# Performance work log

Hardware: AMD Instinct MI355X
Metric: run time of the kernel (lower is better)

## Reference

```python
import jax, jax.numpy as jnp
import numpy as np


def setup_inputs() -> dict:
    key = jax.random.key(0)
    k1, k2 = jax.random.split(key)
    B, C, N = 8, 64, 65536
    features = jax.random.normal(k1, (B, C, N), dtype=jnp.float32)
    coords = jax.random.uniform(k2, (B, 3, N), dtype=jnp.float32)  # normalized xyz in [0,1)
    return {"features": features, "coords": coords, "resolution": 32}


def reference(features, coords, resolution):
    """avg_voxelize: quantize coords to an r^3 grid, scatter-average features.

    features: [B, C, N] float; coords: [B, 3, N] float in [0,1].
    Returns (vox [B, C, r, r, r], norm_coords [B, 3, N]).
    """
    r = resolution
    B, C, N = features.shape
    norm_coords = jnp.clip(coords * r, 0, r - 1)                 # [B, 3, N]
    vox = jnp.round(norm_coords).astype(jnp.int32)               # [B, 3, N]
    # linear voxel index per point: x*r^2 + y*r + z
    idx = (vox[:, 0] * r + vox[:, 1]) * r + vox[:, 2]            # [B, N]
    flat_idx = (idx + jnp.arange(B, dtype=jnp.int32)[:, None] * (r * r * r)).reshape(-1)  # [B*N]
    feats = features.transpose(0, 2, 1).reshape(B * N, C)        # [B*N, C]
    num_seg = B * r * r * r
    sums = jax.ops.segment_sum(feats, flat_idx, num_segments=num_seg)            # [B*r^3, C]
    cnt = jax.ops.segment_sum(jnp.ones((B * N,), features.dtype), flat_idx,
                              num_segments=num_seg)                              # [B*r^3]
    avg = sums / jnp.maximum(cnt, 1.0)[:, None]
    out = avg.reshape(B, r, r, r, C).transpose(0, 4, 1, 2, 3)    # [B, C, r, r, r]
    return out, norm_coords
```

## Files before the change

kernel.cpp:

```cpp
#include <hip/hip_runtime.h>
#include <hip/hip_bf16.h>


#define BB 8
#define CC 64
#define NN 65536
#define RR 32
#define R3 (RR * RR * RR)
#define OFFSTRIDE (R3 + 1)

__global__ __launch_bounds__(256) void points_kernel(
    const float* __restrict__ coords,
    float* __restrict__ norm_out,
    unsigned int* __restrict__ cnt,
    unsigned int* __restrict__ packed)
{
    int gid = blockIdx.x * 256 + threadIdx.x;
    int b = gid >> 16;
    int n = gid & (NN - 1);

    const float* cb = coords + (size_t)b * 3 * NN;
    float x = cb[n];
    float y = cb[NN + n];
    float z = cb[2 * NN + n];

    float nx = fminf(fmaxf(x * (float)RR, 0.0f), (float)(RR - 1));
    float ny = fminf(fmaxf(y * (float)RR, 0.0f), (float)(RR - 1));
    float nz = fminf(fmaxf(z * (float)RR, 0.0f), (float)(RR - 1));

    float* nb = norm_out + (size_t)b * 3 * NN;
    nb[n] = nx;
    nb[NN + n] = ny;
    nb[2 * NN + n] = nz;

    int vx = (int)rintf(nx);
    int vy = (int)rintf(ny);
    int vz = (int)rintf(nz);
    unsigned int idx = (unsigned int)((vx * RR + vy) * RR + vz);

    unsigned int rank = atomicAdd(&cnt[b * R3 + idx], 1u);
    packed[gid] = (idx << 17) | rank;
}

__global__ __launch_bounds__(1024) void scan_kernel(
    const unsigned int* __restrict__ cnt,
    unsigned int* __restrict__ off)
{
    int b = blockIdx.x;
    int t = threadIdx.x;
    const unsigned int* c = cnt + (size_t)b * R3;
    unsigned int* o = off + (size_t)b * OFFSTRIDE;

    unsigned int loc[32];
    unsigned int s = 0;
    #pragma unroll
    for (int k = 0; k < 32; k++) { loc[k] = c[t * 32 + k]; s += loc[k]; }

    __shared__ unsigned int aux[1024];
    aux[t] = s;
    __syncthreads();
    for (int d = 1; d < 1024; d <<= 1) {
        unsigned int v = (t >= d) ? aux[t - d] : 0u;
        __syncthreads();
        aux[t] += v;
        __syncthreads();
    }
    unsigned int run = (t == 0) ? 0u : aux[t - 1];
    #pragma unroll
    for (int k = 0; k < 32; k++) { o[t * 32 + k] = run; run += loc[k]; }
    if (t == 1023) o[R3] = run;
}

__global__ __launch_bounds__(256) void pos_kernel(
    const unsigned int* __restrict__ packed,
    const unsigned int* __restrict__ off,
    unsigned int* __restrict__ pos)
{
    int gid = blockIdx.x * 256 + threadIdx.x;
    int b = gid >> 16;
    unsigned int pk = packed[gid];
    unsigned int ix = pk >> 17;
    unsigned int rk = pk & 0x1FFFFu;
    pos[gid] = off[(size_t)b * OFFSTRIDE + ix] + rk;
}

__global__ __launch_bounds__(1024) void gather_kernel(
    const float* __restrict__ feats,
    const unsigned int* __restrict__ pos,
    const unsigned int* __restrict__ off,
    float* __restrict__ out)
{
    __shared__ __hip_bfloat16 srt[NN];

    int c = blockIdx.x;
    int b = blockIdx.y;
    int t = threadIdx.x;

    const float* f = feats + ((size_t)b * CC + c) * NN;
    const unsigned int* P = pos + (size_t)b * NN;

    for (int n0 = t * 4; n0 < NN; n0 += 1024 * 4) {
        float4 fv = *(const float4*)(f + n0);
        uint4 pv = *(const uint4*)(P + n0);
        srt[pv.x] = __float2bfloat16(fv.x);
        srt[pv.y] = __float2bfloat16(fv.y);
        srt[pv.z] = __float2bfloat16(fv.z);
        srt[pv.w] = __float2bfloat16(fv.w);
    }
    __syncthreads();

    const unsigned int* O = off + (size_t)b * OFFSTRIDE;
    float* ob = out + ((size_t)b * CC + c) * R3;
    for (int j = 0; j < 32; j++) {
        int v = t + j * 1024;
        unsigned int s0 = O[v];
        unsigned int s1 = O[v + 1];
        float s = 0.0f;
        for (unsigned int p = s0; p < s1; p++) s += __bfloat162float(srt[p]);
        float cf = (float)(s1 - s0);
        ob[v] = s / fmaxf(cf, 1.0f);
    }
}

extern "C" void kernel_launch(void* const* d_in, const int* in_sizes, int n_in,
                              void* d_out, int out_size, void* d_ws, size_t ws_size,
                              hipStream_t stream) {
    const float* feats  = (const float*)d_in[0];
    const float* coords = (const float*)d_in[1];

    float* out_vox  = (float*)d_out;
    float* out_norm = out_vox + (size_t)BB * CC * R3;

    char* ws = (char*)d_ws;
    unsigned int* cnt    = (unsigned int*)ws;
    unsigned int* off    = (unsigned int*)(ws + 1048576);
    unsigned int* packed = (unsigned int*)(ws + 1048576 + 1048608);
    unsigned int* pos    = (unsigned int*)(ws + 1048576 + 1048608 + 2097152);

    hipMemsetAsync(cnt, 0, (size_t)BB * R3 * sizeof(unsigned int), stream);

    points_kernel<<<(BB * NN) / 256, 256, 0, stream>>>(coords, out_norm, cnt, packed);
    scan_kernel<<<BB, 1024, 0, stream>>>(cnt, off);
    pos_kernel<<<(BB * NN) / 256, 256, 0, stream>>>(packed, off, pos);
    gather_kernel<<<dim3(CC, BB), 1024, 0, stream>>>(feats, pos, off, out_vox);
}
```

Baseline: 289.3 us.

## Replace counting-sort pipeline with LDS float atomic scatter-add per channel

Drops the scan and position kernels and the sorted bf16 staging buffer. Points now emit 16-bit voxel indices and bump counts, and the gather kernel accumulates features into a 128KB shared float array with unsafe atomic adds before dividing by the counts. The points kernel is also vectorized to four points per thread. This removes two launches and the serial per-voxel loops, and restores fp32 accumulation. In exchange it relies on LDS atomic throughput, and the 128KB shared allocation may limit occupancy to one block per CU.

```diff
diff --git a/kernel.cpp b/kernel.cpp
--- a/kernel.cpp
+++ b/kernel.cpp
@@ -1,5 +1,4 @@
 #include <hip/hip_runtime.h>
-#include <hip/hip_bf16.h>
 
 
 #define BB 8
@@ -7,118 +6,109 @@
 #define NN 65536
 #define RR 32
 #define R3 (RR * RR * RR)
-#define OFFSTRIDE (R3 + 1)
 
 __global__ __launch_bounds__(256) void points_kernel(
     const float* __restrict__ coords,
     float* __restrict__ norm_out,
     unsigned int* __restrict__ cnt,
-    unsigned int* __restrict__ packed)
+    unsigned short* __restrict__ idx_out)
 {
     int gid = blockIdx.x * 256 + threadIdx.x;
-    int b = gid >> 16;
-    int n = gid & (NN - 1);
+    int b  = gid >> 14;
+    int n4 = (gid & 16383) * 4;
 
     const float* cb = coords + (size_t)b * 3 * NN;
-    float x = cb[n];
-    float y = cb[NN + n];
-    float z = cb[2 * NN + n];
+    float4 x = *(const float4*)(cb + n4);
+    float4 y = *(const float4*)(cb + NN + n4);
+    float4 z = *(const float4*)(cb + 2 * NN + n4);
 
-    float nx = fminf(fmaxf(x * (float)RR, 0.0f), (float)(RR - 1));
-    float ny = fminf(fmaxf(y * (float)RR, 0.0f), (float)(RR - 1));
-    float nz = fminf(fmaxf(z * (float)RR, 0.0f), (float)(RR - 1));
+    float4 nx, ny, nz;
+    nx.x = fminf(fmaxf(x.x * 32.f, 0.f), 31.f);
+    nx.y = fminf(fmaxf(x.y * 32.f, 0.f), 31.f);
+    nx.z = fminf(fmaxf(x.z * 32.f, 0.f), 31.f);
+    nx.w = fminf(fmaxf(x.w * 32.f, 0.f), 31.f);
+    ny.x = fminf(fmaxf(y.x * 32.f, 0.f), 31.f);
+    ny.y = fminf(fmaxf(y.y * 32.f, 0.f), 31.f);
+    ny.z = fminf(fmaxf(y.z * 32.f, 0.f), 31.f);
+    ny.w = fminf(fmaxf(y.w * 32.f, 0.f), 31.f);
+    nz.x = fminf(fmaxf(z.x * 32.f, 0.f), 31.f);
+    nz.y = fminf(fmaxf(z.y * 32.f, 0.f), 31.f);
+    nz.z = fminf(fmaxf(z.z * 32.f, 0.f), 31.f);
+    nz.w = fminf(fmaxf(z.w * 32.f, 0.f), 31.f);
 
     float* nb = norm_out + (size_t)b * 3 * NN;
-    nb[n] = nx;
-    nb[NN + n] = ny;
-    nb[2 * NN + n] = nz;
+    *(float4*)(nb + n4)          = nx;
+    *(float4*)(nb + NN + n4)     = ny;
+    *(float4*)(nb + 2 * NN + n4) = nz;
 
-    int vx = (int)rintf(nx);
-    int vy = (int)rintf(ny);
-    int vz = (int)rintf(nz);
-    unsigned int idx = (unsigned int)((vx * RR + vy) * RR + vz);
+    int i0 = ((int)rintf(nx.x) << 10) | ((int)rintf(ny.x) << 5) | (int)rintf(nz.x);
+    int i1 = ((int)rintf(nx.y) << 10) | ((int)rintf(ny.y) << 5) | (int)rintf(nz.y);
+    int i2 = ((int)rintf(nx.z) << 10) | ((int)rintf(ny.z) << 5) | (int)rintf(nz.z);
+    int i3 = ((int)rintf(nx.w) << 10) | ((int)rintf(ny.w) << 5) | (int)rintf(nz.w);
 
-    unsigned int rank = atomicAdd(&cnt[b * R3 + idx], 1u);
-    packed[gid] = (idx << 17) | rank;
-}
+    unsigned short* ib = idx_out + (size_t)b * NN;
+    *(ushort4*)(ib + n4) = make_ushort4((unsigned short)i0, (unsigned short)i1,
+                                        (unsigned short)i2, (unsigned short)i3);
 
-__global__ __launch_bounds__(1024) void scan_kernel(
-    const unsigned int* __restrict__ cnt,
-    unsigned int* __restrict__ off)
-{
-    int b = blockIdx.x;
-    int t = threadIdx.x;
-    const unsigned int* c = cnt + (size_t)b * R3;
-    unsigned int* o = off + (size_t)b * OFFSTRIDE;
-
-    unsigned int loc[32];
-    unsigned int s = 0;
-    #pragma unroll
-    for (int k = 0; k < 32; k++) { loc[k] = c[t * 32 + k]; s += loc[k]; }
-
-    __shared__ unsigned int aux[1024];
-    aux[t] = s;
-    __syncthreads();
-    for (int d = 1; d < 1024; d <<= 1) {
-        unsigned int v = (t >= d) ? aux[t - d] : 0u;
-        __syncthreads();
-        aux[t] += v;
-        __syncthreads();
-    }
-    unsigned int run = (t == 0) ? 0u : aux[t - 1];
-    #pragma unroll
-    for (int k = 0; k < 32; k++) { o[t * 32 + k] = run; run += loc[k]; }
-    if (t == 1023) o[R3] = run;
-}
-
-__global__ __launch_bounds__(256) void pos_kernel(
-    const unsigned int* __restrict__ packed,
-    const unsigned int* __restrict__ off,
-    unsigned int* __restrict__ pos)
-{
-    int gid = blockIdx.x * 256 + threadIdx.x;
-    int b = gid >> 16;
-    unsigned int pk = packed[gid];
-    unsigned int ix = pk >> 17;
-    unsigned int rk = pk & 0x1FFFFu;
-    pos[gid] = off[(size_t)b * OFFSTRIDE + ix] + rk;
+    unsigned int* cc = cnt + (size_t)b * R3;
+    atomicAdd(&cc[i0], 1u);
+    atomicAdd(&cc[i1], 1u);
+    atomicAdd(&cc[i2], 1u);
+    atomicAdd(&cc[i3], 1u);
 }
 
 __global__ __launch_bounds__(1024) void gather_kernel(
     const float* __restrict__ feats,
-    const unsigned int* __restrict__ pos,
-    const unsigned int* __restrict__ off,
+    const unsigned short* __restrict__ idx,
+    const unsigned int* __restrict__ cnt,
     float* __restrict__ out)
 {
-    __shared__ __hip_bfloat16 srt[NN];
+    __shared__ float acc[R3];
 
     int c = blockIdx.x;
     int b = blockIdx.y;
     int t = threadIdx.x;
 
-    const float* f = feats + ((size_t)b * CC + c) * NN;
-    const unsigned int* P = pos + (size_t)b * NN;
-
-    for (int n0 = t * 4; n0 < NN; n0 += 1024 * 4) {
-        float4 fv = *(const float4*)(f + n0);
-        uint4 pv = *(const uint4*)(P + n0);
-        srt[pv.x] = __float2bfloat16(fv.x);
-        srt[pv.y] = __float2bfloat16(fv.y);
-        srt[pv.z] = __float2bfloat16(fv.z);
-        srt[pv.w] = __float2bfloat16(fv.w);
+    #pragma unroll
+    for (int j = 0; j < 8; j++) {
+        *(float4*)(acc + (t + j * 1024) * 4) = make_float4(0.f, 0.f, 0.f, 0.f);
     }
     __syncthreads();
 
-    const unsigned int* O = off + (size_t)b * OFFSTRIDE;
+    const float* f = feats + ((size_t)b * CC + c) * NN;
+    const unsigned short* I = idx + (size_t)b * NN;
+
+    #pragma unroll
+    for (int it = 0; it < 8; it++) {
+        int n0 = (t + it * 1024) * 8;
+        float4 f0 = *(const float4*)(f + n0);
+        float4 f1 = *(const float4*)(f + n0 + 4);
+        ushort4 v0 = *(const ushort4*)(I + n0);
+        ushort4 v1 = *(const ushort4*)(I + n0 + 4);
+        unsafeAtomicAdd(&acc[v0.x], f0.x);
+        unsafeAtomicAdd(&acc[v0.y], f0.y);
+        unsafeAtomicAdd(&acc[v0.z], f0.z);
+        unsafeAtomicAdd(&acc[v0.w], f0.w);
+        unsafeAtomicAdd(&acc[v1.x], f1.x);
+        unsafeAtomicAdd(&acc[v1.y], f1.y);
+        unsafeAtomicAdd(&acc[v1.z], f1.z);
+        unsafeAtomicAdd(&acc[v1.w], f1.w);
+    }
+    __syncthreads();
+
+    const unsigned int* cb = cnt + (size_t)b * R3;
     float* ob = out + ((size_t)b * CC + c) * R3;
-    for (int j = 0; j < 32; j++) {
-        int v = t + j * 1024;
-        unsigned int s0 = O[v];
-        unsigned int s1 = O[v + 1];
-        float s = 0.0f;
-        for (unsigned int p = s0; p < s1; p++) s += __bfloat162float(srt[p]);
-        float cf = (float)(s1 - s0);
-        ob[v] = s / fmaxf(cf, 1.0f);
+    #pragma unroll
+    for (int j = 0; j < 8; j++) {
+        int v = (t + j * 1024) * 4;
+        float4 s = *(const float4*)(acc + v);
+        uint4 cv = *(const uint4*)(cb + v);
+        float4 o;
+        o.x = __fdividef(s.x, fmaxf((float)cv.x, 1.f));
+        o.y = __fdividef(s.y, fmaxf((float)cv.y, 1.f));
+        o.z = __fdividef(s.z, fmaxf((float)cv.z, 1.f));
+        o.w = __fdividef(s.w, fmaxf((float)cv.w, 1.f));
+        *(float4*)(ob + v) = o;
     }
 }
 
@@ -132,15 +122,11 @@
     float* out_norm = out_vox + (size_t)BB * CC * R3;
 
     char* ws = (char*)d_ws;
-    unsigned int* cnt    = (unsigned int*)ws;
-    unsigned int* off    = (unsigned int*)(ws + 1048576);
-    unsigned int* packed = (unsigned int*)(ws + 1048576 + 1048608);
-    unsigned int* pos    = (unsigned int*)(ws + 1048576 + 1048608 + 2097152);
+    unsigned int*   cnt = (unsigned int*)ws;
+    unsigned short* idx = (unsigned short*)(ws + 1048576);
 
     hipMemsetAsync(cnt, 0, (size_t)BB * R3 * sizeof(unsigned int), stream);
 
-    points_kernel<<<(BB * NN) / 256, 256, 0, stream>>>(coords, out_norm, cnt, packed);
-    scan_kernel<<<BB, 1024, 0, stream>>>(cnt, off);
-    pos_kernel<<<(BB * NN) / 256, 256, 0, stream>>>(packed, off, pos);
-    gather_kernel<<<dim3(CC, BB), 1024, 0, stream>>>(feats, pos, off, out_vox);
+    points_kernel<<<(BB * NN / 4) / 256, 256, 0, stream>>>(coords, out_norm, cnt, idx);
+    gather_kernel<<<dim3(CC, BB), 1024, 0, stream>>>(feats, idx, cnt, out_vox);
 }
```

Measured after the change: 363.7 us. +25.7%, slower.

## Replace global atomic histogram with per-block LDS histograms and packed subhistograms

Applied to the files above, without the earlier changes.

Points are binned into per-block shared-memory histograms (4 sub-blocks per batch), and the counts are written as packed 16-bit pairs. This replaces the global atomics and the memset. The scan merges the sub-histograms into per-sub-block prefix offsets, and the pos kernel rewrites packed entries in place, vectorized. The goal is to cut global atomic contention and launch/memset overhead. The trade-off is that points_kernel now runs only 32 blocks, which reduces parallelism in that phase.

```diff
diff --git a/kernel.cpp b/kernel.cpp
--- a/kernel.cpp
+++ b/kernel.cpp
@@ -7,57 +7,110 @@
 #define NN 65536
 #define RR 32
 #define R3 (RR * RR * RR)
-#define OFFSTRIDE (R3 + 1)
-
-__global__ __launch_bounds__(256) void points_kernel(
+#define NSUB 4
+#define PTS (NN / NSUB)
+#define HWORDS (R3 / 2)
+
+__global__ __launch_bounds__(1024) void points_kernel(
     const float* __restrict__ coords,
     float* __restrict__ norm_out,
-    unsigned int* __restrict__ cnt,
-    unsigned int* __restrict__ packed)
-{
-    int gid = blockIdx.x * 256 + threadIdx.x;
-    int b = gid >> 16;
-    int n = gid & (NN - 1);
+    unsigned int* __restrict__ packed,
+    unsigned int* __restrict__ ghist)
+{
+    __shared__ unsigned int hist[R3];
+    int blk = blockIdx.x;
+    int b = blk >> 2;
+    int s = blk & 3;
+    int t = threadIdx.x;
+
+    #pragma unroll
+    for (int k = 0; k < 8; k++)
+        *(uint4*)(hist + 4 * (t + k * 1024)) = make_uint4(0u, 0u, 0u, 0u);
+    __syncthreads();
 
     const float* cb = coords + (size_t)b * 3 * NN;
-    float x = cb[n];
-    float y = cb[NN + n];
-    float z = cb[2 * NN + n];
-
-    float nx = fminf(fmaxf(x * (float)RR, 0.0f), (float)(RR - 1));
-    float ny = fminf(fmaxf(y * (float)RR, 0.0f), (float)(RR - 1));
-    float nz = fminf(fmaxf(z * (float)RR, 0.0f), (float)(RR - 1));
-
     float* nb = norm_out + (size_t)b * 3 * NN;
-    nb[n] = nx;
-    nb[NN + n] = ny;
-    nb[2 * NN + n] = nz;
-
-    int vx = (int)rintf(nx);
-    int vy = (int)rintf(ny);
-    int vz = (int)rintf(nz);
-    unsigned int idx = (unsigned int)((vx * RR + vy) * RR + vz);
-
-    unsigned int rank = atomicAdd(&cnt[b * R3 + idx], 1u);
-    packed[gid] = (idx << 17) | rank;
+    unsigned int* pb = packed + (size_t)b * NN;
+
+    #pragma unroll
+    for (int p = 0; p < 4; p++) {
+        int n = s * PTS + (t + p * 1024) * 4;
+        float4 x = *(const float4*)(cb + n);
+        float4 y = *(const float4*)(cb + NN + n);
+        float4 z = *(const float4*)(cb + 2 * NN + n);
+
+        float4 nx, ny, nz;
+        nx.x = fminf(fmaxf(x.x * 32.f, 0.f), 31.f);
+        nx.y = fminf(fmaxf(x.y * 32.f, 0.f), 31.f);
+        nx.z = fminf(fmaxf(x.z * 32.f, 0.f), 31.f);
+        nx.w = fminf(fmaxf(x.w * 32.f, 0.f), 31.f);
+        ny.x = fminf(fmaxf(y.x * 32.f, 0.f), 31.f);
+        ny.y = fminf(fmaxf(y.y * 32.f, 0.f), 31.f);
+        ny.z = fminf(fmaxf(y.z * 32.f, 0.f), 31.f);
+        ny.w = fminf(fmaxf(y.w * 32.f, 0.f), 31.f);
+        nz.x = fminf(fmaxf(z.x * 32.f, 0.f), 31.f);
+        nz.y = fminf(fmaxf(z.y * 32.f, 0.f), 31.f);
+        nz.z = fminf(fmaxf(z.z * 32.f, 0.f), 31.f);
+        nz.w = fminf(fmaxf(z.w * 32.f, 0.f), 31.f);
+
+        *(float4*)(nb + n)          = nx;
+        *(float4*)(nb + NN + n)     = ny;
+        *(float4*)(nb + 2 * NN + n) = nz;
+
+        int i0 = ((int)rintf(nx.x) << 10) | ((int)rintf(ny.x) << 5) | (int)rintf(nz.x);
+        int i1 = ((int)rintf(nx.y) << 10) | ((int)rintf(ny.y) << 5) | (int)rintf(nz.y);
+        int i2 = ((int)rintf(nx.z) << 10) | ((int)rintf(ny.z) << 5) | (int)rintf(nz.z);
+        int i3 = ((int)rintf(nx.w) << 10) | ((int)rintf(ny.w) << 5) | (int)rintf(nz.w);
+
+        unsigned int r0 = atomicAdd(&hist[i0], 1u);
+        unsigned int r1 = atomicAdd(&hist[i1], 1u);
+        unsigned int r2 = atomicAdd(&hist[i2], 1u);
+        unsigned int r3 = atomicAdd(&hist[i3], 1u);
+
+        *(uint4*)(pb + n) = make_uint4(((unsigned)i0 << 14) | r0,
+                                       ((unsigned)i1 << 14) | r1,
+                                       ((unsigned)i2 << 14) | r2,
+                                       ((unsigned)i3 << 14) | r3);
+    }
+    __syncthreads();
+
+    unsigned int* gh = ghist + (size_t)blk * HWORDS;
+    #pragma unroll
+    for (int k = 0; k < 16; k++) {
+        int w = t + k * 1024;
+        uint2 u = *(const uint2*)(hist + 2 * w);
+        gh[w] = u.x | (u.y << 16);
+    }
 }
 
 __global__ __launch_bounds__(1024) void scan_kernel(
-    const unsigned int* __restrict__ cnt,
+    unsigned int* __restrict__ ghist,
     unsigned int* __restrict__ off)
 {
     int b = blockIdx.x;
     int t = threadIdx.x;
-    const unsigned int* c = cnt + (size_t)b * R3;
-    unsigned int* o = off + (size_t)b * OFFSTRIDE;
-
-    unsigned int loc[32];
-    unsigned int s = 0;
-    #pragma unroll
-    for (int k = 0; k < 32; k++) { loc[k] = c[t * 32 + k]; s += loc[k]; }
+
+    unsigned int cnt_lo[16], cnt_hi[16];
+    unsigned int tsum = 0;
+    #pragma unroll
+    for (int k = 0; k < 16; k++) {
+        int w = t * 16 + k;
+        unsigned int lo = 0, hi = 0;
+        #pragma unroll
+        for (int s = 0; s < NSUB; s++) {
+            unsigned int* p = ghist + (size_t)(b * NSUB + s) * HWORDS + w;
+            unsigned int u = *p;
+            *p = lo | (hi << 16);
+            lo += u & 0xFFFFu;
+            hi += u >> 16;
+        }
+        cnt_lo[k] = lo;
+        cnt_hi[k] = hi;
+        tsum += lo + hi;
+    }
 
     __shared__ unsigned int aux[1024];
-    aux[t] = s;
+    aux[t] = tsum;
     __syncthreads();
     for (int d = 1; d < 1024; d <<= 1) {
         unsigned int v = (t >= d) ? aux[t - d] : 0u;
@@ -66,22 +119,52 @@
         __syncthreads();
     }
     unsigned int run = (t == 0) ? 0u : aux[t - 1];
-    #pragma unroll
-    for (int k = 0; k < 32; k++) { o[t * 32 + k] = run; run += loc[k]; }
-    if (t == 1023) o[R3] = run;
+
+    unsigned int* O = off + (size_t)b * R3;
+    #pragma unroll
+    for (int k = 0; k < 16; k++) {
+        int v = t * 32 + 2 * k;
+        *(uint2*)(O + v) = make_uint2(run, run + cnt_lo[k]);
+        run += cnt_lo[k] + cnt_hi[k];
+    }
 }
 
 __global__ __launch_bounds__(256) void pos_kernel(
-    const unsigned int* __restrict__ packed,
+    unsigned int* __restrict__ packed,
     const unsigned int* __restrict__ off,
-    unsigned int* __restrict__ pos)
+    const unsigned int* __restrict__ ghist)
 {
     int gid = blockIdx.x * 256 + threadIdx.x;
-    int b = gid >> 16;
-    unsigned int pk = packed[gid];
-    unsigned int ix = pk >> 17;
-    unsigned int rk = pk & 0x1FFFFu;
-    pos[gid] = off[(size_t)b * OFFSTRIDE + ix] + rk;
+    int b  = gid >> 14;
+    int n4 = (gid & 16383) * 4;
+    int s  = n4 >> 14;
+
+    unsigned int* pb = packed + (size_t)b * NN + n4;
+    const unsigned int* O = off + (size_t)b * R3;
+    const unsigned int* G = ghist + (size_t)(b * NSUB + s) * HWORDS;
+
+    uint4 pk = *(uint4*)pb;
+    {
+        unsigned v = pk.x >> 14, r = pk.x & 16383u;
+        unsigned u = G[v >> 1];
+        pk.x = O[v] + ((v & 1) ? (u >> 16) : (u & 0xFFFFu)) + r;
+    }
+    {
+        unsigned v = pk.y >> 14, r = pk.y & 16383u;
+        unsigned u = G[v >> 1];
+        pk.y = O[v] + ((v & 1) ? (u >> 16) : (u & 0xFFFFu)) + r;
+    }
+    {
+        unsigned v = pk.z >> 14, r = pk.z & 16383u;
+        unsigned u = G[v >> 1];
+        pk.z = O[v] + ((v & 1) ? (u >> 16) : (u & 0xFFFFu)) + r;
+    }
+    {
+        unsigned v = pk.w >> 14, r = pk.w & 16383u;
+        unsigned u = G[v >> 1];
+        pk.w = O[v] + ((v & 1) ? (u >> 16) : (u & 0xFFFFu)) + r;
+    }
+    *(uint4*)pb = pk;
 }
 
 __global__ __launch_bounds__(1024) void gather_kernel(
@@ -109,16 +192,15 @@
     }
     __syncthreads();
 
-    const unsigned int* O = off + (size_t)b * OFFSTRIDE;
+    const unsigned int* O = off + (size_t)b * R3;
     float* ob = out + ((size_t)b * CC + c) * R3;
     for (int j = 0; j < 32; j++) {
         int v = t + j * 1024;
         unsigned int s0 = O[v];
-        unsigned int s1 = O[v + 1];
+        unsigned int s1 = (v < R3 - 1) ? O[v + 1] : (unsigned)NN;
         float s = 0.0f;
         for (unsigned int p = s0; p < s1; p++) s += __bfloat162float(srt[p]);
-        float cf = (float)(s1 - s0);
-        ob[v] = s / fmaxf(cf, 1.0f);
+        ob[v] = __fdividef(s, fmaxf((float)(s1 - s0), 1.0f));
     }
 }
 
@@ -132,15 +214,12 @@
     float* out_norm = out_vox + (size_t)BB * CC * R3;
 
     char* ws = (char*)d_ws;
-    unsigned int* cnt    = (unsigned int*)ws;
-    unsigned int* off    = (unsigned int*)(ws + 1048576);
-    unsigned int* packed = (unsigned int*)(ws + 1048576 + 1048608);
-    unsigned int* pos    = (unsigned int*)(ws + 1048576 + 1048608 + 2097152);
-
-    hipMemsetAsync(cnt, 0, (size_t)BB * R3 * sizeof(unsigned int), stream);
-
-    points_kernel<<<(BB * NN) / 256, 256, 0, stream>>>(coords, out_norm, cnt, packed);
-    scan_kernel<<<BB, 1024, 0, stream>>>(cnt, off);
-    pos_kernel<<<(BB * NN) / 256, 256, 0, stream>>>(packed, off, pos);
-    gather_kernel<<<dim3(CC, BB), 1024, 0, stream>>>(feats, pos, off, out_vox);
-}
+    unsigned int* ghist  = (unsigned int*)ws;
+    unsigned int* packed = (unsigned int*)(ws + (2 << 20));
+    unsigned int* off    = (unsigned int*)(ws + (4 << 20));
+
+    points_kernel<<<BB * NSUB, 1024, 0, stream>>>(coords, out_norm, packed, ghist);
+    scan_kernel<<<BB, 1024, 0, stream>>>(ghist, off);
+    pos_kernel<<<(BB * NN / 4) / 256, 256, 0, stream>>>(packed, off, ghist);
+    gather_kernel<<<dim3(CC, BB), 1024, 0, stream>>>(feats, packed, off, out_vox);
+}
```

After: 286.9 us. No clear change (-0.9%).
